# Kernel optimization log

Hardware: AMD Instinct MI355X
Metric: run time of the kernel (lower is better)

The kernel has to match this reference:

```python
import jax, jax.numpy as jnp
import numpy as np

MAX_SEQ_LEN = 1000

def _ln(x, g, b, eps=1e-5):
    m = jnp.mean(x, -1, keepdims=True)
    v = jnp.var(x, -1, keepdims=True)
    return (x - m) * jax.lax.rsqrt(v + eps) * g + b

def _conv1d(x, k, b):
    # x [B,T,Cin], k [K,Cin,Cout], 'SAME' padding (odd kernel)
    return jax.lax.conv_general_dilated(x, k, (1,), 'SAME', dimension_numbers=('NWC', 'WIO', 'NWC')) + b

def _dwconv(x, w):
    # lightweight conv: softmax-normalized depthwise kernel, w [C,K]
    k = jnp.transpose(jax.nn.softmax(w, axis=1))[:, None, :]  # [K,1,C]
    return jax.lax.conv_general_dilated(x, k, (1,), 'SAME', dimension_numbers=('NWC', 'WIO', 'NWC'), feature_group_count=x.shape[-1])

def _conv2d(x, k, b):
    # x [B,H,W,Cin], k [kh,kw,Cin,Cout]
    return jax.lax.conv_general_dilated(x, k, (1, 1), 'SAME', dimension_numbers=('NHWC', 'HWIO', 'NHWC')) + b

def _lconv(x, mask, ln_g, ln_b, glu_w, glu_b, dw, out_w, out_b):
    # LConvBlock: LN -> GLU projection -> depthwise lightweight conv -> out proj -> residual, masked
    res = x
    h = _ln(x, ln_g, ln_b)
    h = h @ glu_w + glu_b
    a, g = jnp.split(h, 2, axis=-1)
    h = a * jax.nn.sigmoid(g)
    h = jnp.where(mask[..., None], 0.0, h)
    h = _dwconv(h, dw)
    h = h @ out_w + out_b
    h = h + res
    return jnp.where(mask[..., None], 0.0, h)

def _forward(content_embedding, speaker_embedding_B, rhythm_B, scaled_duration_outputs,
             in_w, in_b,
             lc0_ln_g, lc0_ln_b, lc0_glu_w, lc0_glu_b, lc0_dw, lc0_out_w, lc0_out_b,
             lc1_ln_g, lc1_ln_b, lc1_glu_w, lc1_glu_b, lc1_dw, lc1_out_w, lc1_out_b,
             p1_w, p1_b, p2_k, p2_b,
             cw_k, cw_b, cw_ln_g, cw_ln_b,
             mkb1_k, mkb1_b, mkb2_k, mkb2_b,
             lw_w, lw_b, ln_g, ln_b, text_mask):
    B, S, _ = content_embedding.shape
    spk = jnp.broadcast_to(speaker_embedding_B[:, None, :], (B, S, speaker_embedding_B.shape[-1]))
    x = jnp.concatenate([content_embedding, spk], -1) @ in_w + in_b
    # duration predictor
    V = _lconv(x, text_mask, lc0_ln_g, lc0_ln_b, lc0_glu_w, lc0_glu_b, lc0_dw, lc0_out_w, lc0_out_b)
    V = _lconv(V, text_mask, lc1_ln_g, lc1_ln_b, lc1_glu_w, lc1_glu_b, lc1_dw, lc1_out_w, lc1_out_b)
    D = jax.nn.softplus(V @ p1_w + p1_b)[..., 0]
    D = jnp.where(text_mask, 0.0, D)
    T = _conv1d(V, p2_k, p2_b)  # [B,S,upsampled_dim]
    # learnable upsampling
    pred_phoneme_len = scaled_duration_outputs.sum(-1)
    alpha_B = jax.lax.stop_gradient(pred_phoneme_len / rhythm_B) / D.sum(-1)
    sD = alpha_B[:, None] * D
    sV = alpha_B[:, None, None] * V
    sT = alpha_B[:, None, None] * T
    mel_len = jnp.clip(jnp.round(sD.sum(-1)).astype(jnp.int32), 1, MAX_SEQ_LEN)
    mel_mask = jnp.arange(MAX_SEQ_LEN)[None, :] >= mel_len[:, None]  # True = pad
    attn_mask = mel_mask[:, :, None] & text_mask[:, None, :]  # bmm(mel_mask, src_mask^T).bool()
    e_k = jnp.cumsum(sD, axis=1)
    s_k = e_k - sD
    t = jnp.arange(1, MAX_SEQ_LEN + 1, dtype=sD.dtype)[None, :, None]
    Sm = jnp.where(attn_mask, 0.0, t - s_k[:, None, :])
    Em = jnp.where(attn_mask, 0.0, e_k[:, None, :] - t)
    # conv_w block: conv1d -> relu -> LN
    Cv = _ln(jax.nn.relu(_conv1d(sV, cw_k, cw_b)), cw_ln_g, cw_ln_b)  # [B,S,CW]
    feat = jnp.concatenate([Sm[..., None], Em[..., None],
                            jnp.broadcast_to(Cv[:, None, :, :], (B, MAX_SEQ_LEN, S, Cv.shape[-1]))], -1)
    h = jax.nn.silu(_conv2d(feat, mkb1_k, mkb1_b))
    h = jax.nn.silu(_conv2d(h, mkb2_k, mkb2_b))
    Wsc = (h @ lw_w + lw_b)[..., 0]  # [B,mel,S]
    Wsc = jnp.where(attn_mask | text_mask[:, None, :], -jnp.inf, Wsc)
    Wmat = jax.nn.softmax(Wsc, axis=2)
    up = jnp.matmul(Wmat, sT)
    up = _ln(up, ln_g, ln_b)
    up = jnp.where(mel_mask[..., None], 0.0, up)
    return up, Wmat, alpha_B, mel_len, mel_mask

def setup_inputs() -> dict:
    key = jax.random.key(0)
    ks = iter(jax.random.split(key, 64))
    B, S, DC, DS, H, CW, MKB, K = 8, 256, 192, 64, 256, 16, 16, 3
    def w(shape, scale=0.02):
        return jax.random.normal(next(ks), shape, jnp.float32) * scale
    inp = {}
    inp['content_embedding'] = jax.random.normal(next(ks), (B, S, DC), jnp.float32)
    inp['speaker_embedding_B'] = jax.random.normal(next(ks), (B, DS), jnp.float32)
    inp['rhythm_B'] = 0.15 + 0.1 * jax.random.uniform(next(ks), (B,), jnp.float32)
    inp['scaled_duration_outputs'] = jax.random.uniform(next(ks), (B, S), jnp.float32)
    lens = jax.random.randint(next(ks), (B,), 200, S + 1)
    inp['text_mask'] = jnp.arange(S)[None, :] >= lens[:, None]
    inp['in_w'] = w((DC + DS, H)); inp['in_b'] = jnp.zeros((H,), jnp.float32)
    for i in range(2):
        inp[f'lc{i}_ln_g'] = jnp.ones((H,), jnp.float32); inp[f'lc{i}_ln_b'] = jnp.zeros((H,), jnp.float32)
        inp[f'lc{i}_glu_w'] = w((H, 2 * H)); inp[f'lc{i}_glu_b'] = jnp.zeros((2 * H,), jnp.float32)
        inp[f'lc{i}_dw'] = w((H, K), 1.0)
        inp[f'lc{i}_out_w'] = w((H, H)); inp[f'lc{i}_out_b'] = jnp.zeros((H,), jnp.float32)
    inp['p1_w'] = w((H, 1)); inp['p1_b'] = jnp.zeros((1,), jnp.float32)
    inp['p2_k'] = w((K, H, H)); inp['p2_b'] = jnp.zeros((H,), jnp.float32)
    inp['cw_k'] = w((K, H, CW)); inp['cw_b'] = jnp.zeros((CW,), jnp.float32)
    inp['cw_ln_g'] = jnp.ones((CW,), jnp.float32); inp['cw_ln_b'] = jnp.zeros((CW,), jnp.float32)
    inp['mkb1_k'] = w((K, K, CW + 2, MKB)); inp['mkb1_b'] = jnp.zeros((MKB,), jnp.float32)
    inp['mkb2_k'] = w((K, K, MKB, MKB)); inp['mkb2_b'] = jnp.zeros((MKB,), jnp.float32)
    inp['lw_w'] = w((MKB, 1)); inp['lw_b'] = jnp.zeros((1,), jnp.float32)
    inp['ln_g'] = jnp.ones((H,), jnp.float32); inp['ln_b'] = jnp.zeros((H,), jnp.float32)
    return inp

def reference(content_embedding, speaker_embedding_B, rhythm_B, scaled_duration_outputs,
              text_mask,
              in_w, in_b,
              lc0_ln_g, lc0_ln_b, lc0_glu_w, lc0_glu_b, lc0_dw, lc0_out_w, lc0_out_b,
              lc1_ln_g, lc1_ln_b, lc1_glu_w, lc1_glu_b, lc1_dw, lc1_out_w, lc1_out_b,
              p1_w, p1_b, p2_k, p2_b,
              cw_k, cw_b, cw_ln_g, cw_ln_b,
              mkb1_k, mkb1_b, mkb2_k, mkb2_b,
              lw_w, lw_b, ln_g, ln_b):
    return _forward(content_embedding, speaker_embedding_B, rhythm_B, scaled_duration_outputs,
                    in_w, in_b,
                    lc0_ln_g, lc0_ln_b, lc0_glu_w, lc0_glu_b, lc0_dw, lc0_out_w, lc0_out_b,
                    lc1_ln_g, lc1_ln_b, lc1_glu_w, lc1_glu_b, lc1_dw, lc1_out_w, lc1_out_b,
                    p1_w, p1_b, p2_k, p2_b,
                    cw_k, cw_b, cw_ln_g, cw_ln_b,
                    mkb1_k, mkb1_b, mkb2_k, mkb2_b,
                    lw_w, lw_b, ln_g, ln_b, text_mask)
```

## Files before the change

kernel.cpp:

```cpp
#include <hip/hip_runtime.h>
#include <math.h>

#define SS 256
#define HH 256
#define MLEN 1000
#define CWW 16
#define NOC 16
#define RB 24

typedef __attribute__((ext_vector_type(8))) short bfrag;
typedef __attribute__((ext_vector_type(4))) float ffrag;

#define WS_V2     1048576u
#define WS_STT    1835008u
#define WS_WB     2097152u
#define WS_CCV    2424832u
#define WS_SSV    2457600u
#define WS_CCI    2490368u
#define WS_SSI    2523136u
#define WS_CP     2555904u
#define WS_CV     2654208u
#define WS_EK     2686976u
#define WS_SK     2689024u
#define WS_ALPHA  2691072u
#define WS_MELI   2691080u
#define WS_TMASK  2691088u

#define PK_IN     0u
#define PK_GLU0   65536u
#define PK_GLU1   196608u
#define PK_OUT0   327680u
#define PK_OUT1   393216u
#define PK_P2     458752u

#define OUT_UP    0u
#define OUT_W     2048000u
#define OUT_ALPHA 4096000u
#define OUT_MLEN  4096008u
#define OUT_MMASK 4096016u

__device__ __forceinline__ unsigned bf16rne(float x){
  unsigned u=__float_as_uint(x);
  u += 0x7fffu + ((u>>16)&1u);
  return u;
}
__device__ __forceinline__ unsigned short bf16h(float x){ return (unsigned short)(bf16rne(x)>>16); }
__device__ __forceinline__ float bf2f(unsigned short u){ return __uint_as_float(((unsigned)u)<<16); }
__device__ __forceinline__ unsigned frag_idx(int k,int n,int KT){
  return (unsigned)(((((n>>4)*KT+(k>>5))*64 + ((k>>3)&3)*16 + (n&15))<<3) + (k&7));
}

__global__ __launch_bounds__(256) void k_prepmask(const void* __restrict__ traw,
    const float* __restrict__ in_w,
    const float* __restrict__ g0, const float* __restrict__ g1,
    const float* __restrict__ o0, const float* __restrict__ o1,
    const float* __restrict__ p2k, float* __restrict__ ws){
  int tid=threadIdx.x;
  if(blockIdx.x==256){
    __shared__ int s_fu, s_ff, s_nz;
    const unsigned char* mb=(const unsigned char*)traw;
    const unsigned int*  mw=(const unsigned int*)traw;
    if(tid==0){s_fu=0;s_ff=0;s_nz=0;}
    __syncthreads();
    int fu=0,ff=0,nz=0;
    for(int w=tid;w<512;w+=256){
      unsigned int v=mw[w];
      if(v){ nz=1; if(v==0x3F800000u) ff=1; else if(v&0xFFFFFF00u) fu=1; }
    }
    if(fu) atomicOr(&s_fu,1);
    if(ff) atomicOr(&s_ff,1);
    if(nz) atomicOr(&s_nz,1);
    __syncthreads();
    int words = (s_ff || (!s_fu && s_nz));
    for(int i=tid;i<2048;i+=256){
      unsigned int v = words ? mw[i] : (unsigned int)mb[i];
      ws[WS_TMASK+i] = v ? 1.0f : 0.0f;
    }
    return;
  }
  unsigned short* wb=(unsigned short*)(ws+WS_WB);
  int gid=blockIdx.x*256+tid, stride=65536;
  for(int i=gid;i<65536;i+=stride){ int k=i>>8,n=i&255; wb[PK_IN  +frag_idx(k,n,8)]=bf16h(in_w[i]); }
  for(int i=gid;i<131072;i+=stride){ int k=i>>9,n=i&511; wb[PK_GLU0+frag_idx(k,n,8)]=bf16h(g0[i]); }
  for(int i=gid;i<131072;i+=stride){ int k=i>>9,n=i&511; wb[PK_GLU1+frag_idx(k,n,8)]=bf16h(g1[i]); }
  for(int i=gid;i<65536;i+=stride){ int k=i>>8,n=i&255; wb[PK_OUT0+frag_idx(k,n,8)]=bf16h(o0[i]); }
  for(int i=gid;i<65536;i+=stride){ int k=i>>8,n=i&255; wb[PK_OUT1+frag_idx(k,n,8)]=bf16h(o1[i]); }
  for(int i=gid;i<196608;i+=stride){ int k3=i>>16,r=i&65535,k=r>>8,n=r&255;
    wb[PK_P2+(unsigned)k3*65536u+frag_idx(k,n,8)]=bf16h(p2k[i]); }
}

__global__ __launch_bounds__(256) void k_front(
    const float* __restrict__ ce, const float* __restrict__ spk,
    const unsigned short* __restrict__ wb, const float* __restrict__ in_b,
    const float* __restrict__ g0b, const float* __restrict__ ln0g, const float* __restrict__ ln0b,
    const float* __restrict__ dw0, const float* __restrict__ o0b,
    const float* __restrict__ g1b, const float* __restrict__ ln1g, const float* __restrict__ ln1b,
    const float* __restrict__ dw1, const float* __restrict__ o1b,
    const float* __restrict__ tmask, float* __restrict__ V2){
  __shared__ unsigned short Abf[16][264];
  __shared__ unsigned short Hb[8][264];
  __shared__ float Xf[8][264];
  __shared__ float Vf[8][264];
  __shared__ float dws[2][3][256];
  __shared__ float tmL[8];
  int b=blockIdx.x>>6, tile=blockIdx.x&63, s0=tile*4, tid=threadIdx.x;
  int w=tid>>6, lane=tid&63, lq=lane>>4, lm=lane&15;
  {
    float d0=dw0[tid*3],d1=dw0[tid*3+1],d2=dw0[tid*3+2];
    float mx=fmaxf(d0,fmaxf(d1,d2));
    float e0=__expf(d0-mx),e1=__expf(d1-mx),e2=__expf(d2-mx);
    float inv=1.0f/(e0+e1+e2);
    dws[0][0][tid]=e0*inv; dws[0][1][tid]=e1*inv; dws[0][2][tid]=e2*inv;
    d0=dw1[tid*3];d1=dw1[tid*3+1];d2=dw1[tid*3+2];
    mx=fmaxf(d0,fmaxf(d1,d2));
    e0=__expf(d0-mx);e1=__expf(d1-mx);e2=__expf(d2-mx);
    inv=1.0f/(e0+e1+e2);
    dws[1][0][tid]=e0*inv; dws[1][1][tid]=e1*inv; dws[1][2][tid]=e2*inv;
  }
  if(tid<8){
    int sI=s0-2+tid;
    tmL[tid]=(sI>=0&&sI<256)? tmask[b*256+sI] : 1.0f;
  }
  for(int it=0;it<8;it++){
    float v=0.f;
    int sI=s0-2+it;
    if(sI>=0 && sI<256){
      int m=b*256+sI;
      v=(tid<192)? ce[m*192+tid] : spk[b*64+tid-192];
    }
    Abf[it][tid]=bf16h(v);
  }
  for(int it=8;it<16;it++) Abf[it][tid]=0;
  __syncthreads();
  {
    ffrag acc[4];
    #pragma unroll
    for(int j=0;j<4;j++){acc[j][0]=0;acc[j][1]=0;acc[j][2]=0;acc[j][3]=0;}
    #pragma unroll
    for(int kt=0;kt<8;kt++){
      bfrag af=*(const bfrag*)&Abf[lm][kt*32+lq*8];
      #pragma unroll
      for(int j=0;j<4;j++){
        int nt=w*4+j;
        bfrag bf=*(const bfrag*)(wb+PK_IN+((((unsigned)(nt*8+kt))*64u+(unsigned)lane)<<3));
        acc[j]=__builtin_amdgcn_mfma_f32_16x16x32_bf16(af,bf,acc[j],0,0,0);
      }
    }
    #pragma unroll
    for(int j=0;j<4;j++){
      int n=w*64+j*16+lm;
      float bn=in_b[n];
      #pragma unroll
      for(int reg=0;reg<4;reg++){
        int row=lq*4+reg;
        if(row<8) Xf[row][n]=acc[j][reg]+bn;
      }
    }
  }
  __syncthreads();
  {
    int r=tid>>4, seg=tid&15;
    if(r<8){
      float s=0.f,q=0.f;
      #pragma unroll
      for(int j4=0;j4<4;j4++){
        float4 v=*(const float4*)&Xf[r][seg*16+j4*4];
        s+=v.x+v.y+v.z+v.w; q+=v.x*v.x+v.y*v.y+v.z*v.z+v.w*v.w;
      }
      s+=__shfl_xor(s,1); q+=__shfl_xor(q,1);
      s+=__shfl_xor(s,2); q+=__shfl_xor(q,2);
      s+=__shfl_xor(s,4); q+=__shfl_xor(q,4);
      s+=__shfl_xor(s,8); q+=__shfl_xor(q,8);
      float mean=s*(1.0f/256.0f), rstd=rsqrtf(q*(1.0f/256.0f)-mean*mean+1e-5f);
      #pragma unroll
      for(int j4=0;j4<4;j4++){
        int c=seg*16+j4*4;
        float4 v=*(const float4*)&Xf[r][c];
        unsigned short q0=bf16h((v.x-mean)*rstd*ln0g[c+0]+ln0b[c+0]);
        unsigned short q1=bf16h((v.y-mean)*rstd*ln0g[c+1]+ln0b[c+1]);
        unsigned short q2=bf16h((v.z-mean)*rstd*ln0g[c+2]+ln0b[c+2]);
        unsigned short q3=bf16h((v.w-mean)*rstd*ln0g[c+3]+ln0b[c+3]);
        *(uint2*)&Abf[r][c]=make_uint2((unsigned)q0|((unsigned)q1<<16),(unsigned)q2|((unsigned)q3<<16));
      }
    }
  }
  __syncthreads();
  {
    ffrag aa[4],ag[4];
    #pragma unroll
    for(int j=0;j<4;j++){aa[j][0]=0;aa[j][1]=0;aa[j][2]=0;aa[j][3]=0;
                         ag[j][0]=0;ag[j][1]=0;ag[j][2]=0;ag[j][3]=0;}
    #pragma unroll
    for(int kt=0;kt<8;kt++){
      bfrag af=*(const bfrag*)&Abf[lm][kt*32+lq*8];
      #pragma unroll
      for(int j=0;j<4;j++){
        int nta=w*4+j, ntg=nta+16;
        bfrag bfa=*(const bfrag*)(wb+PK_GLU0+((((unsigned)(nta*8+kt))*64u+(unsigned)lane)<<3));
        bfrag bfg=*(const bfrag*)(wb+PK_GLU0+((((unsigned)(ntg*8+kt))*64u+(unsigned)lane)<<3));
        aa[j]=__builtin_amdgcn_mfma_f32_16x16x32_bf16(af,bfa,aa[j],0,0,0);
        ag[j]=__builtin_amdgcn_mfma_f32_16x16x32_bf16(af,bfg,ag[j],0,0,0);
      }
    }
    __syncthreads();
    #pragma unroll
    for(int j=0;j<4;j++){
      int n=w*64+j*16+lm;
      float ba=g0b[n], bg=g0b[n+256];
      #pragma unroll
      for(int reg=0;reg<4;reg++){
        int row=lq*4+reg;
        if(row<8){
          float a=aa[j][reg]+ba, g=ag[j][reg]+bg;
          float hv=a*(1.0f/(1.0f+__expf(-g)));
          if(tmL[row]!=0.0f) hv=0.0f;
          Hb[row][n]=bf16h(hv);
        }
      }
    }
  }
  __syncthreads();
  {
    float w0=dws[0][0][tid],w1=dws[0][1][tid],w2=dws[0][2][tid];
    for(int r=0;r<6;r++){
      float a=w0*bf2f(Hb[r][tid])+w1*bf2f(Hb[r+1][tid])+w2*bf2f(Hb[r+2][tid]);
      Abf[r][tid]=bf16h(a);
    }
    Abf[6][tid]=0; Abf[7][tid]=0;
  }
  __syncthreads();
  {
    ffrag acc[4];
    #pragma unroll
    for(int j=0;j<4;j++){acc[j][0]=0;acc[j][1]=0;acc[j][2]=0;acc[j][3]=0;}
    #pragma unroll
    for(int kt=0;kt<8;kt++){
      bfrag af=*(const bfrag*)&Abf[lm][kt*32+lq*8];
      #pragma unroll
      for(int j=0;j<4;j++){
        int nt=w*4+j;
        bfrag bf=*(const bfrag*)(wb+PK_OUT0+((((unsigned)(nt*8+kt))*64u+(unsigned)lane)<<3));
        acc[j]=__builtin_amdgcn_mfma_f32_16x16x32_bf16(af,bf,acc[j],0,0,0);
      }
    }
    #pragma unroll
    for(int j=0;j<4;j++){
      int n=w*64+j*16+lm;
      float bn=o0b[n];
      #pragma unroll
      for(int reg=0;reg<4;reg++){
        int row=lq*4+reg;
        if(row<6){
          float v=(tmL[row+1]==0.0f)? acc[j][reg]+bn+Xf[row+1][n] : 0.0f;
          Vf[row][n]=v;
        }
      }
    }
  }
  __syncthreads();
  {
    int r=tid>>4, seg=tid&15;
    if(r<6){
      float s=0.f,q=0.f;
      #pragma unroll
      for(int j4=0;j4<4;j4++){
        float4 v=*(const float4*)&Vf[r][seg*16+j4*4];
        s+=v.x+v.y+v.z+v.w; q+=v.x*v.x+v.y*v.y+v.z*v.z+v.w*v.w;
      }
      s+=__shfl_xor(s,1); q+=__shfl_xor(q,1);
      s+=__shfl_xor(s,2); q+=__shfl_xor(q,2);
      s+=__shfl_xor(s,4); q+=__shfl_xor(q,4);
      s+=__shfl_xor(s,8); q+=__shfl_xor(q,8);
      float mean=s*(1.0f/256.0f), rstd=rsqrtf(q*(1.0f/256.0f)-mean*mean+1e-5f);
      #pragma unroll
      for(int j4=0;j4<4;j4++){
        int c=seg*16+j4*4;
        float4 v=*(const float4*)&Vf[r][c];
        unsigned short q0=bf16h((v.x-mean)*rstd*ln1g[c+0]+ln1b[c+0]);
        unsigned short q1=bf16h((v.y-mean)*rstd*ln1g[c+1]+ln1b[c+1]);
        unsigned short q2=bf16h((v.z-mean)*rstd*ln1g[c+2]+ln1b[c+2]);
        unsigned short q3=bf16h((v.w-mean)*rstd*ln1g[c+3]+ln1b[c+3]);
        *(uint2*)&Abf[r][c]=make_uint2((unsigned)q0|((unsigned)q1<<16),(unsigned)q2|((unsigned)q3<<16));
      }
    }
  }
  __syncthreads();
  {
    ffrag aa[4],ag[4];
    #pragma unroll
    for(int j=0;j<4;j++){aa[j][0]=0;aa[j][1]=0;aa[j][2]=0;aa[j][3]=0;
                         ag[j][0]=0;ag[j][1]=0;ag[j][2]=0;ag[j][3]=0;}
    #pragma unroll
    for(int kt=0;kt<8;kt++){
      bfrag af=*(const bfrag*)&Abf[lm][kt*32+lq*8];
      #pragma unroll
      for(int j=0;j<4;j++){
        int nta=w*4+j, ntg=nta+16;
        bfrag bfa=*(const bfrag*)(wb+PK_GLU1+((((unsigned)(nta*8+kt))*64u+(unsigned)lane)<<3));
        bfrag bfg=*(const bfrag*)(wb+PK_GLU1+((((unsigned)(ntg*8+kt))*64u+(unsigned)lane)<<3));
        aa[j]=__builtin_amdgcn_mfma_f32_16x16x32_bf16(af,bfa,aa[j],0,0,0);
        ag[j]=__builtin_amdgcn_mfma_f32_16x16x32_bf16(af,bfg,ag[j],0,0,0);
      }
    }
    __syncthreads();
    #pragma unroll
    for(int j=0;j<4;j++){
      int n=w*64+j*16+lm;
      float ba=g1b[n], bg=g1b[n+256];
      #pragma unroll
      for(int reg=0;reg<4;reg++){
        int row=lq*4+reg;
        if(row<6){
          float a=aa[j][reg]+ba, g=ag[j][reg]+bg;
          float hv=a*(1.0f/(1.0f+__expf(-g)));
          if(tmL[row+1]!=0.0f) hv=0.0f;
          Hb[row][n]=bf16h(hv);
        }
      }
    }
  }
  __syncthreads();
  {
    float w0=dws[1][0][tid],w1=dws[1][1][tid],w2=dws[1][2][tid];
    for(int r=0;r<4;r++){
      float a=w0*bf2f(Hb[r][tid])+w1*bf2f(Hb[r+1][tid])+w2*bf2f(Hb[r+2][tid]);
      Abf[r][tid]=bf16h(a);
    }
    Abf[4][tid]=0; Abf[5][tid]=0;
  }
  __syncthreads();
  {
    ffrag acc[4];
    #pragma unroll
    for(int j=0;j<4;j++){acc[j][0]=0;acc[j][1]=0;acc[j][2]=0;acc[j][3]=0;}
    #pragma unroll
    for(int kt=0;kt<8;kt++){
      bfrag af=*(const bfrag*)&Abf[lm][kt*32+lq*8];
      #pragma unroll
      for(int j=0;j<4;j++){
        int nt=w*4+j;
        bfrag bf=*(const bfrag*)(wb+PK_OUT1+((((unsigned)(nt*8+kt))*64u+(unsigned)lane)<<3));
        acc[j]=__builtin_amdgcn_mfma_f32_16x16x32_bf16(af,bf,acc[j],0,0,0);
      }
    }
    #pragma unroll
    for(int j=0;j<4;j++){
      int n=w*64+j*16+lm;
      float bn=o1b[n];
      #pragma unroll
      for(int reg=0;reg<4;reg++){
        int row=lq*4+reg;
        if(row<4){
          float v=(tmL[row+2]!=0.0f)? 0.0f : acc[j][reg]+bn+Vf[row+1][n];
          V2[(unsigned)(b*256+s0+row)*256u+n]=v;
        }
      }
    }
  }
}

__global__ __launch_bounds__(256) void k_dur(const float* __restrict__ V2, const float* __restrict__ p1w,
    const float* __restrict__ p1b, const float* __restrict__ sdo, const float* __restrict__ rhythm,
    float* __restrict__ ws, float* __restrict__ outp){
  __shared__ float p1[HH];
  __shared__ float sd[SS];
  __shared__ float red[16];
  int b=blockIdx.x, tid=threadIdx.x;
  int wid=tid>>6, lane=tid&63;
  p1[tid]=p1w[tid];
  __syncthreads();
  float accd=p1b[0];
  const float* row=V2+(unsigned)(b*SS+tid)*HH;
  for(int k=0;k<HH;k+=4){
    float4 v=*(const float4*)&row[k];
    accd+=v.x*p1[k]+v.y*p1[k+1]+v.z*p1[k+2]+v.w*p1[k+3];
  }
  float Dv=fmaxf(accd,0.0f)+log1pf(expf(-fabsf(accd)));
  if(ws[WS_TMASK+b*SS+tid]!=0.0f) Dv=0.0f;
  float sv=sdo[b*SS+tid];
  float a=Dv, c=sv;
  for(int off=32;off;off>>=1){ a+=__shfl_down(a,off); c+=__shfl_down(c,off); }
  if(lane==0){ red[wid]=a; red[wid+8]=c; }
  __syncthreads();
  float Dsum=red[0]+red[1]+red[2]+red[3];
  float pred=red[8]+red[9]+red[10]+red[11];
  float al=(pred/rhythm[b])/Dsum;
  float sDv=al*Dv;
  sd[tid]=sDv;
  __syncthreads();
  for(int off=1;off<SS;off<<=1){
    float t=(tid>=off)?sd[tid-off]:0.0f;
    __syncthreads();
    sd[tid]+=t;
    __syncthreads();
  }
  float ek=sd[tid], sk=ek-sDv;
  ws[WS_EK+b*SS+tid]=ek;
  ws[WS_SK+b*SS+tid]=sk;
  float melf=sd[SS-1];
  int mel=(int)rintf(melf); mel=mel<1?1:(mel>MLEN?MLEN:mel);
  if(tid==0){
    ws[WS_ALPHA+b]=al;
    ((int*)ws)[WS_MELI+b]=mel;
    outp[OUT_ALPHA+b]=al;
    outp[OUT_MLEN+b]=(float)mel;
  }
  for(int t=tid;t<MLEN;t+=SS) outp[OUT_MMASK+b*MLEN+t]=(t>=mel)?1.0f:0.0f;
}

__global__ __launch_bounds__(256) void k_post(const float* __restrict__ V2,
    const unsigned short* __restrict__ wbp2, const float* __restrict__ p2b,
    const float* __restrict__ cwk, const float* __restrict__ cwb,
    const float* __restrict__ cwg, const float* __restrict__ cwbe,
    float* __restrict__ ws){
  int bx=blockIdx.x, tid=threadIdx.x;
  if(bx<256){
    __shared__ unsigned short Abf[18][264];
    int m0=(bx>>1)*16, nh=bx&1, b=m0>>8, s0=m0&255;
    for(int it=0;it<18;it++){
      int sI=s0-1+it;
      float v=(sI>=0&&sI<256)? V2[(unsigned)(b*256+sI)*256u+tid] : 0.0f;
      Abf[it][tid]=bf16h(v);
    }
    __syncthreads();
    int w=tid>>6, lane=tid&63, lq=lane>>4, lm=lane&15;
    ffrag acc[2];
    #pragma unroll
    for(int tt=0;tt<2;tt++){ acc[tt][0]=0;acc[tt][1]=0;acc[tt][2]=0;acc[tt][3]=0; }
    for(int k3=0;k3<3;k3++){
      const unsigned short* wb3=wbp2+(unsigned)k3*65536u;
      #pragma unroll
      for(int kt=0;kt<8;kt++){
        bfrag af=*(const bfrag*)&Abf[lm+k3][kt*32+lq*8];
        #pragma unroll
        for(int tt=0;tt<2;tt++){
          int nt=nh*8+w*2+tt;
          bfrag bf=*(const bfrag*)(wb3+((((unsigned)(nt*8+kt))*64u+(unsigned)lane)<<3));
          acc[tt]=__builtin_amdgcn_mfma_f32_16x16x32_bf16(af,bf,acc[tt],0,0,0);
        }
      }
    }
    float al=ws[WS_ALPHA+b];
    unsigned short* stt=(unsigned short*)(ws+WS_STT);
    #pragma unroll
    for(int tt=0;tt<2;tt++){
      int n=nh*128+w*32+tt*16+lm;
      float bn=p2b[n];
      unsigned short o0=bf16h((acc[tt][0]+bn)*al);
      unsigned short o1=bf16h((acc[tt][1]+bn)*al);
      unsigned short o2=bf16h((acc[tt][2]+bn)*al);
      unsigned short o3=bf16h((acc[tt][3]+bn)*al);
      *(uint2*)&stt[((unsigned)(b*256+n)<<8)+(unsigned)(s0+lq*4)]=
        make_uint2((unsigned)o0|((unsigned)o1<<16),(unsigned)o2|((unsigned)o3<<16));
    }
  } else {
    __shared__ float Vt[18][SS];
    int bb=bx-256;
    int b=bb>>4, tile=bb&15;
    int sbase=tile*16;
    float al=ws[WS_ALPHA+b];
    for(int rr=0;rr<18;rr++){
      int s=sbase-1+rr;
      Vt[rr][tid]=(s>=0&&s<SS)?al*V2[(b*SS+s)*HH+tid]:0.0f;
    }
    __syncthreads();
    int sl=tid>>4, oc=tid&15;
    float a0=cwb[oc],a1=0.f,a2=0.f,a3=0.f;
    for(int k3=0;k3<3;k3++){
      const float* vp=&Vt[sl+k3][0];
      const float* wpp=cwk+(unsigned)k3*HH*CWW+oc;
      for(int c=0;c<HH;c+=4){
        a0+=vp[c+0]*wpp[(c+0)*CWW];
        a1+=vp[c+1]*wpp[(c+1)*CWW];
        a2+=vp[c+2]*wpp[(c+2)*CWW];
        a3+=vp[c+3]*wpp[(c+3)*CWW];
      }
    }
    float acc=fmaxf((a0+a1)+(a2+a3),0.0f);
    float ssum=acc, qsum=acc*acc;
    for(int off=8;off;off>>=1){ ssum+=__shfl_xor(ssum,off); qsum+=__shfl_xor(qsum,off); }
    float mean=ssum*(1.0f/CWW), var=qsum*(1.0f/CWW)-mean*mean;
    float cv=(acc-mean)*rsqrtf(var+1e-5f)*cwg[oc]+cwbe[oc];
    ws[WS_CV+(unsigned)(b*SS+sbase+sl)*CWW+oc]=cv;
  }
}

__global__ __launch_bounds__(256) void k_cp(const float* __restrict__ mkb1k, const float* __restrict__ mkb1b,
    float* __restrict__ ws){
  __shared__ float CvL[258][17];
  __shared__ float k1c[3][3][CWW][NOC];
  __shared__ float kab[3][3][2][NOC];
  __shared__ float skE[258], ekE[258], fiE[258];
  int b=blockIdx.x, tid=threadIdx.x;
  for(int i=tid;i<3*3*CWW*NOC;i+=256){
    int oc=i&15, ic=(i>>4)&15, kk=i>>8;
    int kw=kk%3, kh=kk/3;
    k1c[kh][kw][ic][oc]=mkb1k[((kh*3+kw)*18+2+ic)*NOC+oc];
  }
  for(int i=tid;i<3*3*2*NOC;i+=256){
    int oc=i&15, ch=(i>>4)&1, kk=i>>5;
    int kw=kk%3, kh=kk/3;
    kab[kh][kw][ch][oc]=mkb1k[((kh*3+kw)*18+ch)*NOC+oc];
  }
  for(int i=tid;i<SS*CWW;i+=256) CvL[1+(i>>4)][i&15]=ws[WS_CV+(unsigned)b*SS*CWW+i];
  if(tid<CWW){ CvL[0][tid]=0.f; CvL[257][tid]=0.f; }
  if(tid<258){
    float sk=0.f, ek=0.f, fi=0.f;
    if(tid>=1 && tid<=SS){
      sk=ws[WS_SK+b*SS+tid-1];
      ek=ws[WS_EK+b*SS+tid-1];
      fi=(ws[WS_TMASK+b*SS+tid-1]!=0.0f)?0.0f:1.0f;
    }
    skE[tid]=sk; ekE[tid]=ek; fiE[tid]=fi;
  }
  __syncthreads();
  float* cpg=ws+WS_CP+(unsigned)b*3*SS*NOC;
  float ccv[16],ssv[16],cci[16],ssi[16];
  #pragma unroll
  for(int oc=0;oc<NOC;oc++){ float bb2=mkb1b[oc]; ccv[oc]=bb2; cci[oc]=bb2; ssv[oc]=0.f; ssi[oc]=0.f; }
  for(int dt=0;dt<3;dt++){
    float acc[NOC];
    #pragma unroll
    for(int oc=0;oc<NOC;oc++) acc[oc]=0.f;
    #pragma unroll
    for(int ds=0;ds<3;ds++){
      #pragma unroll
      for(int ic=0;ic<CWW;ic++){
        float v=CvL[tid+ds][ic];
        #pragma unroll
        for(int oc=0;oc<NOC;oc++) acc[oc]+=v*k1c[dt][ds][ic][oc];
      }
    }
    for(int oc=0;oc<NOC;oc++) cpg[(unsigned)(dt*SS+tid)*NOC+oc]=acc[oc];
    float va[16],vb[16],ia[16],ib2[16];
    #pragma unroll
    for(int oc=0;oc<NOC;oc++){ va[oc]=0.f; vb[oc]=0.f; ia[oc]=0.f; ib2[oc]=0.f; }
    #pragma unroll
    for(int ds=0;ds<3;ds++){
      int j=tid+ds;
      float inb=(j>=1&&j<=SS)?1.0f:0.0f;
      float fb=fiE[j];
      float skv=skE[j], ekv=ekE[j];
      #pragma unroll
      for(int oc=0;oc<NOC;oc++){
        float ka=kab[dt][ds][0][oc], kb=kab[dt][ds][1][oc];
        float d=ka-kb, e=kb*ekv-ka*skv;
        va[oc]+=inb*d; vb[oc]+=inb*e; ia[oc]+=fb*d; ib2[oc]+=fb*e;
      }
    }
    float dtf=(float)dt;
    #pragma unroll
    for(int oc=0;oc<NOC;oc++){
      ccv[oc]+=acc[oc]+vb[oc]+dtf*va[oc]; ssv[oc]+=va[oc];
      cci[oc]+=acc[oc]+ib2[oc]+dtf*ia[oc]; ssi[oc]+=ia[oc];
    }
  }
  unsigned base=(unsigned)(b*SS+tid)*16u;
  for(int oc=0;oc<NOC;oc++){
    ws[WS_CCV+base+oc]=ccv[oc];
    ws[WS_SSV+base+oc]=ssv[oc];
    ws[WS_CCI+base+oc]=cci[oc];
    ws[WS_SSI+base+oc]=ssi[oc];
  }
}

__global__ __launch_bounds__(256,4) void k_stageB(
    const float* __restrict__ ws, const float* __restrict__ mkb1k, const float* __restrict__ mkb1b,
    const float* __restrict__ mkb2k, const float* __restrict__ mkb2b,
    const float* __restrict__ lww, const float* __restrict__ lwb,
    float* __restrict__ outp){
  __shared__ short ringh[3][258][RB];
  __shared__ float skL[258], ekL[258];
  __shared__ unsigned char finC[260];
  __shared__ __align__(16) float wscL[SS];
  __shared__ float red[16];
  int bx=blockIdx.x, b=bx/125, chunk=bx%125, t0=chunk*8, tid=threadIdx.x;
  int wid=tid>>6, lane=tid&63;
  int lq=lane>>4, lm=lane&15;
  if(tid<258){
    float sk=0.f, ek=0.f; unsigned char fin=0;
    if(tid>=1 && tid<=SS){
      sk=ws[WS_SK+b*SS+tid-1];
      ek=ws[WS_EK+b*SS+tid-1];
      fin=(ws[WS_TMASK+b*SS+tid-1]!=0.0f)?0:1;
    }
    skL[tid]=sk; ekL[tid]=ek; finC[tid]=fin;
  }
  if(tid<72){
    int sl=tid/24, rem=tid%24;
    int row=(rem<12)?0:257, c=(rem%12)*2;
    *(int*)&ringh[sl][row][c]=0;
  }
  int mel=((const int*)ws)[WS_MELI+b];
  __syncthreads();

  const float* cpb=ws+WS_CP+(unsigned)b*3*SS*NOC;

  unsigned offA[5]; int dtL[5], zgL[5];
  bfrag bfw[5];
  {
    #pragma unroll
    for(int i=0;i<5;i++){
      int g=4*i+lq;
      int dt,ds,hf,zg;
      if(g<18){ dt=g/6; int rm=g-6*dt; ds=rm>>1; hf=rm&1; zg=0; }
      else { dt=0; ds=0; hf=0; zg=1; }
      int srow=wid*64+lm+ds;
      offA[i]=(unsigned)((srow*RB+8*hf)*2);
      dtL[i]=dt; zgL[i]=zg;
      int pk[4];
      if(!zg){
        #pragma unroll
        for(int j=0;j<4;j++){
          unsigned u0=bf16rne(mkb2k[(8*g+2*j)*NOC+lm]);
          unsigned u1=bf16rne(mkb2k[(8*g+2*j+1)*NOC+lm]);
          pk[j]=(int)((u0>>16)|(u1&0xffff0000u));
        }
      } else pk[0]=pk[1]=pk[2]=pk[3]=0;
      bfw[i]=__builtin_bit_cast(bfrag, make_int4(pk[0],pk[1],pk[2],pk[3]));
    }
  }
  float b2v=mkb2b[lm];
  float lwwv=lww[lm];
  float lwb0=lwb[0];
  const char* ringB=(const char*)&ringh[0][0][0];
  bfrag azero={};

  auto conv1row=[&](int T){
    int s=tid;
    float acc[NOC];
    bool fv=(T>=1)&&(T<=998)&&(T+1<mel);
    bool fi=(T>=2)&&(T<=998)&&(T-1>=mel);
    if(fv||fi){
      const float* cc=ws+(fv?WS_CCV:WS_CCI)+(unsigned)(b*SS+s)*16u;
      const float* s2=ws+(fv?WS_SSV:WS_SSI)+(unsigned)(b*SS+s)*16u;
      float Tf=(float)T;
      #pragma unroll
      for(int q=0;q<4;q++){
        float4 c4=((const float4*)cc)[q];
        float4 s4=((const float4*)s2)[q];
        acc[4*q+0]=c4.x+Tf*s4.x; acc[4*q+1]=c4.y+Tf*s4.y;
        acc[4*q+2]=c4.z+Tf*s4.z; acc[4*q+3]=c4.w+Tf*s4.w;
      }
    } else {
      #pragma unroll
      for(int oc=0;oc<NOC;oc++) acc[oc]=mkb1b[oc];
      #pragma unroll
      for(int dt=0;dt<3;dt++){
        int tr=T+dt-1;
        if(tr<0||tr>=MLEN) continue;
        bool valid=(tr<mel);
        float tt=(float)(tr+1);
        float gg[3], hh[3];
        #pragma unroll
        for(int ds=0;ds<3;ds++){
          int j=s+ds;
          float f = valid ? ((j>=1&&j<=SS)?1.0f:0.0f) : (float)finC[j];
          gg[ds]=f*(tt-skL[j]);
          hh[ds]=f*(ekL[j]-tt);
        }
        const float* cpr=cpb+(unsigned)(dt*SS+s)*NOC;
        float4 c0=((const float4*)cpr)[0], c1=((const float4*)cpr)[1];
        float4 c2=((const float4*)cpr)[2], c3=((const float4*)cpr)[3];
        acc[0]+=c0.x; acc[1]+=c0.y; acc[2]+=c0.z; acc[3]+=c0.w;
        acc[4]+=c1.x; acc[5]+=c1.y; acc[6]+=c1.z; acc[7]+=c1.w;
        acc[8]+=c2.x; acc[9]+=c2.y; acc[10]+=c2.z; acc[11]+=c2.w;
        acc[12]+=c3.x; acc[13]+=c3.y; acc[14]+=c3.z; acc[15]+=c3.w;
        #pragma unroll
        for(int ds=0;ds<3;ds++){
          const float* kA=mkb1k+((dt*3+ds)*18+0)*NOC;
          const float* kB=mkb1k+((dt*3+ds)*18+1)*NOC;
          #pragma unroll
          for(int oc=0;oc<NOC;oc++) acc[oc]+=gg[ds]*kA[oc]+hh[ds]*kB[oc];
        }
      }
    }
    int slot=T%3;
    int pk[8];
    #pragma unroll
    for(int j=0;j<8;j++){
      float x0=acc[2*j], x1=acc[2*j+1];
      float s0=x0/(1.0f+__expf(-x0));
      float s1=x1/(1.0f+__expf(-x1));
      unsigned u0=bf16rne(s0), u1=bf16rne(s1);
      pk[j]=(int)((u0>>16)|(u1&0xffff0000u));
    }
    int4* dst=(int4*)&ringh[slot][s+1][0];
    dst[0]=make_int4(pk[0],pk[1],pk[2],pk[3]);
    dst[1]=make_int4(pk[4],pk[5],pk[6],pk[7]);
  };

  if(t0>0) conv1row(t0-1);
  conv1row(t0);

  #pragma unroll 1
  for(int r=0;r<8;r++){
    int t=t0+r;
    if(t+1<MLEN) conv1row(t+1);
    __syncthreads();
    int tmod=t%3;
    ffrag acc2[4];
    #pragma unroll
    for(int tt=0;tt<4;tt++){ acc2[tt][0]=b2v; acc2[tt][1]=b2v; acc2[tt][2]=b2v; acc2[tt][3]=b2v; }
    #pragma unroll
    for(int i=0;i<5;i++){
      int dt=dtL[i];
      int x=tmod+dt+2; x=(x>=3)?x-3:x; x=(x>=3)?x-3:x;
      int tr=t+dt-1;
      bool av=((unsigned)tr<(unsigned)MLEN)&&(!zgL[i]);
      const char* rp=ringB+(unsigned)x*(258u*RB*2u)+offA[i];
      #pragma unroll
      for(int tt=0;tt<4;tt++){
        int4 ra=*(const int4*)(rp+tt*(16*RB*2));
        bfrag a=av?__builtin_bit_cast(bfrag,ra):azero;
        acc2[tt]=__builtin_amdgcn_mfma_f32_16x16x32_bf16(a,bfw[i],acc2[tt],0,0,0);
      }
    }
    #pragma unroll
    for(int tt=0;tt<4;tt++){
      float out4[4];
      #pragma unroll
      for(int q=0;q<4;q++){
        float xx=acc2[tt][q];
        float pv=(xx/(1.0f+__expf(-xx)))*lwwv;
        pv+=__shfl_xor(pv,1); pv+=__shfl_xor(pv,2); pv+=__shfl_xor(pv,4); pv+=__shfl_xor(pv,8);
        out4[q]=pv+lwb0;
      }
      if(lm==0){
        *(float4*)&wscL[wid*64+tt*16+lq*4]=make_float4(out4[0],out4[1],out4[2],out4[3]);
      }
    }
    __syncthreads();
    float fm=(float)finC[tid+1];
    float wsc=wscL[tid];
    float val=(fm!=0.0f)?wsc:-3.0e38f;
    float mx=val;
    for(int off=32;off;off>>=1) mx=fmaxf(mx,__shfl_down(mx,off));
    if(lane==0) red[wid]=mx;
    __syncthreads();
    mx=fmaxf(fmaxf(red[0],red[1]),fmaxf(red[2],red[3]));
    float e=(fm!=0.0f)?__expf(wsc-mx):0.0f;
    float sm=e;
    for(int off=32;off;off>>=1) sm+=__shfl_down(sm,off);
    if(lane==0) red[8+wid]=sm;
    __syncthreads();
    sm=red[8]+red[9]+red[10]+red[11];
    outp[OUT_W+(unsigned)(b*MLEN+t)*SS+tid]=e/sm;
    __syncthreads();
  }
}

__global__ __launch_bounds__(256) void k_up(const float* __restrict__ ws,
    const float* __restrict__ lng, const float* __restrict__ lnb, float* __restrict__ outp){
  __shared__ unsigned short Wbf[16][264];
  __shared__ float UpL[16][264];
  __shared__ float gb[2][256];
  int bx=blockIdx.x, b=bx/63, tile=bx%63, t0=tile*16, tid=threadIdx.x;
  gb[0][tid]=lng[tid]; gb[1][tid]=lnb[tid];
  for(int it=0;it<16;it++){
    int t=t0+it;
    float v=(t<MLEN)? outp[OUT_W+(unsigned)(b*MLEN+t)*256u+tid] : 0.0f;
    Wbf[it][tid]=bf16h(v);
  }
  int mel=((const int*)ws)[WS_MELI+b];
  __syncthreads();
  int w=tid>>6, lane=tid&63, lq=lane>>4, lm=lane&15;
  const unsigned short* stt=(const unsigned short*)(ws+WS_STT)+(unsigned)b*65536u;
  ffrag acc[4];
  #pragma unroll
  for(int tt=0;tt<4;tt++){ acc[tt][0]=0;acc[tt][1]=0;acc[tt][2]=0;acc[tt][3]=0; }
  #pragma unroll
  for(int kt=0;kt<8;kt++){
    bfrag af=*(const bfrag*)&Wbf[lm][kt*32+lq*8];
    #pragma unroll
    for(int tt=0;tt<4;tt++){
      int n=w*64+tt*16+lm;
      bfrag bf=*(const bfrag*)(stt+((unsigned)n<<8)+(unsigned)(kt*32+lq*8));
      acc[tt]=__builtin_amdgcn_mfma_f32_16x16x32_bf16(af,bf,acc[tt],0,0,0);
    }
  }
  #pragma unroll
  for(int tt=0;tt<4;tt++){
    #pragma unroll
    for(int reg=0;reg<4;reg++)
      UpL[lq*4+reg][w*64+tt*16+lm]=acc[tt][reg];
  }
  __syncthreads();
  int r=tid>>4, seg=tid&15;
  float s=0.f,q=0.f;
  #pragma unroll
  for(int j4=0;j4<4;j4++){
    float4 v=*(const float4*)&UpL[r][seg*16+j4*4];
    s+=v.x+v.y+v.z+v.w; q+=v.x*v.x+v.y*v.y+v.z*v.z+v.w*v.w;
  }
  s+=__shfl_xor(s,1); q+=__shfl_xor(q,1);
  s+=__shfl_xor(s,2); q+=__shfl_xor(q,2);
  s+=__shfl_xor(s,4); q+=__shfl_xor(q,4);
  s+=__shfl_xor(s,8); q+=__shfl_xor(q,8);
  float mean=s*(1.0f/256.0f), rstd=rsqrtf(q*(1.0f/256.0f)-mean*mean+1e-5f);
  int t=t0+r;
  if(t<MLEN){
    bool vld=(t<mel);
    #pragma unroll
    for(int j4=0;j4<4;j4++){
      int c=seg*16+j4*4;
      float4 v=*(const float4*)&UpL[r][c];
      float4 o;
      o.x=vld?((v.x-mean)*rstd*gb[0][c+0]+gb[1][c+0]):0.0f;
      o.y=vld?((v.y-mean)*rstd*gb[0][c+1]+gb[1][c+1]):0.0f;
      o.z=vld?((v.z-mean)*rstd*gb[0][c+2]+gb[1][c+2]):0.0f;
      o.w=vld?((v.w-mean)*rstd*gb[0][c+3]+gb[1][c+3]):0.0f;
      *(float4*)&outp[OUT_UP+(unsigned)(b*MLEN+t)*256u+c]=o;
    }
  }
}

extern "C" void kernel_launch(void* const* d_in, const int* in_sizes, int n_in,
                              void* d_out, int out_size, void* d_ws, size_t ws_size,
                              hipStream_t stream){
  const float* ce   =(const float*)d_in[0];
  const float* spk  =(const float*)d_in[1];
  const float* rhy  =(const float*)d_in[2];
  const float* sdo  =(const float*)d_in[3];
  const void*  tmr  =d_in[4];
  const float* in_w =(const float*)d_in[5];
  const float* in_b =(const float*)d_in[6];
  const float* l0lg =(const float*)d_in[7];
  const float* l0lb =(const float*)d_in[8];
  const float* l0gw =(const float*)d_in[9];
  const float* l0gb =(const float*)d_in[10];
  const float* l0dw =(const float*)d_in[11];
  const float* l0ow =(const float*)d_in[12];
  const float* l0ob =(const float*)d_in[13];
  const float* l1lg =(const float*)d_in[14];
  const float* l1lb =(const float*)d_in[15];
  const float* l1gw =(const float*)d_in[16];
  const float* l1gb =(const float*)d_in[17];
  const float* l1dw =(const float*)d_in[18];
  const float* l1ow =(const float*)d_in[19];
  const float* l1ob =(const float*)d_in[20];
  const float* p1w  =(const float*)d_in[21];
  const float* p1b  =(const float*)d_in[22];
  const float* p2k  =(const float*)d_in[23];
  const float* p2b  =(const float*)d_in[24];
  const float* cwk  =(const float*)d_in[25];
  const float* cwb  =(const float*)d_in[26];
  const float* cwg  =(const float*)d_in[27];
  const float* cwbe =(const float*)d_in[28];
  const float* m1k  =(const float*)d_in[29];
  const float* m1b  =(const float*)d_in[30];
  const float* m2k  =(const float*)d_in[31];
  const float* m2b  =(const float*)d_in[32];
  const float* lww  =(const float*)d_in[33];
  const float* lwbp =(const float*)d_in[34];
  const float* lng  =(const float*)d_in[35];
  const float* lnb  =(const float*)d_in[36];
  float* ws=(float*)d_ws;
  float* outp=(float*)d_out;
  const unsigned short* wbb=(const unsigned short*)(ws+WS_WB);

  k_prepmask<<<257,256,0,stream>>>(tmr, in_w, l0gw, l1gw, l0ow, l1ow, p2k, ws);
  k_front   <<<512,256,0,stream>>>(ce, spk, wbb, in_b,
                                   l0gb, l0lg, l0lb, l0dw, l0ob,
                                   l1gb, l1lg, l1lb, l1dw, l1ob,
                                   ws+WS_TMASK, ws+WS_V2);
  k_dur     <<<8,256,0,stream>>>(ws+WS_V2, p1w, p1b, sdo, rhy, ws, outp);
  k_post    <<<384,256,0,stream>>>(ws+WS_V2, wbb+PK_P2, p2b, cwk, cwb, cwg, cwbe, ws);
  k_cp      <<<8,256,0,stream>>>(m1k, m1b, ws);
  k_stageB  <<<1000,256,0,stream>>>(ws, m1k, m1b, m2k, m2b, lww, lwbp, outp);
  k_up      <<<504,256,0,stream>>>(ws, lng, lnb, outp);
}
```

Before: 324.5 us.

## Fuse duration, post-projection and upsampling kernels by deferring alpha scaling

Alpha depends on the duration sums, but it only scales linear conv outputs, so its application is moved later. That lets the duration predictor run as extra blocks inside the post-projection kernel, with the bias, ReLU and LayerNorm of the conv channel moved into k_cp. The upsampling GEMM and its LayerNorm are fused into the tail of k_stageB, reusing its ring shared memory. This removes two launches and a serial dependency, but the 16-row MFMA now uses only 8 valid rows and stageB gains more shared memory and longer blocks.

```diff
diff --git a/kernel.cpp b/kernel.cpp
--- a/kernel.cpp
+++ b/kernel.cpp
@@ -359,60 +359,12 @@
   }
 }
 
-__global__ __launch_bounds__(256) void k_dur(const float* __restrict__ V2, const float* __restrict__ p1w,
-    const float* __restrict__ p1b, const float* __restrict__ sdo, const float* __restrict__ rhythm,
+__global__ __launch_bounds__(256) void k_postdur(const float* __restrict__ V2,
+    const unsigned short* __restrict__ wbp2, const float* __restrict__ p2b,
+    const float* __restrict__ cwk,
+    const float* __restrict__ p1w, const float* __restrict__ p1b,
+    const float* __restrict__ sdo, const float* __restrict__ rhythm,
     float* __restrict__ ws, float* __restrict__ outp){
-  __shared__ float p1[HH];
-  __shared__ float sd[SS];
-  __shared__ float red[16];
-  int b=blockIdx.x, tid=threadIdx.x;
-  int wid=tid>>6, lane=tid&63;
-  p1[tid]=p1w[tid];
-  __syncthreads();
-  float accd=p1b[0];
-  const float* row=V2+(unsigned)(b*SS+tid)*HH;
-  for(int k=0;k<HH;k+=4){
-    float4 v=*(const float4*)&row[k];
-    accd+=v.x*p1[k]+v.y*p1[k+1]+v.z*p1[k+2]+v.w*p1[k+3];
-  }
-  float Dv=fmaxf(accd,0.0f)+log1pf(expf(-fabsf(accd)));
-  if(ws[WS_TMASK+b*SS+tid]!=0.0f) Dv=0.0f;
-  float sv=sdo[b*SS+tid];
-  float a=Dv, c=sv;
-  for(int off=32;off;off>>=1){ a+=__shfl_down(a,off); c+=__shfl_down(c,off); }
-  if(lane==0){ red[wid]=a; red[wid+8]=c; }
-  __syncthreads();
-  float Dsum=red[0]+red[1]+red[2]+red[3];
-  float pred=red[8]+red[9]+red[10]+red[11];
-  float al=(pred/rhythm[b])/Dsum;
-  float sDv=al*Dv;
-  sd[tid]=sDv;
-  __syncthreads();
-  for(int off=1;off<SS;off<<=1){
-    float t=(tid>=off)?sd[tid-off]:0.0f;
-    __syncthreads();
-    sd[tid]+=t;
-    __syncthreads();
-  }
-  float ek=sd[tid], sk=ek-sDv;
-  ws[WS_EK+b*SS+tid]=ek;
-  ws[WS_SK+b*SS+tid]=sk;
-  float melf=sd[SS-1];
-  int mel=(int)rintf(melf); mel=mel<1?1:(mel>MLEN?MLEN:mel);
-  if(tid==0){
-    ws[WS_ALPHA+b]=al;
-    ((int*)ws)[WS_MELI+b]=mel;
-    outp[OUT_ALPHA+b]=al;
-    outp[OUT_MLEN+b]=(float)mel;
-  }
-  for(int t=tid;t<MLEN;t+=SS) outp[OUT_MMASK+b*MLEN+t]=(t>=mel)?1.0f:0.0f;
-}
-
-__global__ __launch_bounds__(256) void k_post(const float* __restrict__ V2,
-    const unsigned short* __restrict__ wbp2, const float* __restrict__ p2b,
-    const float* __restrict__ cwk, const float* __restrict__ cwb,
-    const float* __restrict__ cwg, const float* __restrict__ cwbe,
-    float* __restrict__ ws){
   int bx=blockIdx.x, tid=threadIdx.x;
   if(bx<256){
     __shared__ unsigned short Abf[18][264];
@@ -440,32 +392,30 @@
         }
       }
     }
-    float al=ws[WS_ALPHA+b];
     unsigned short* stt=(unsigned short*)(ws+WS_STT);
     #pragma unroll
     for(int tt=0;tt<2;tt++){
       int n=nh*128+w*32+tt*16+lm;
       float bn=p2b[n];
-      unsigned short o0=bf16h((acc[tt][0]+bn)*al);
-      unsigned short o1=bf16h((acc[tt][1]+bn)*al);
-      unsigned short o2=bf16h((acc[tt][2]+bn)*al);
-      unsigned short o3=bf16h((acc[tt][3]+bn)*al);
+      unsigned short o0=bf16h(acc[tt][0]+bn);
+      unsigned short o1=bf16h(acc[tt][1]+bn);
+      unsigned short o2=bf16h(acc[tt][2]+bn);
+      unsigned short o3=bf16h(acc[tt][3]+bn);
       *(uint2*)&stt[((unsigned)(b*256+n)<<8)+(unsigned)(s0+lq*4)]=
         make_uint2((unsigned)o0|((unsigned)o1<<16),(unsigned)o2|((unsigned)o3<<16));
     }
-  } else {
+  } else if(bx<384){
     __shared__ float Vt[18][SS];
     int bb=bx-256;
     int b=bb>>4, tile=bb&15;
     int sbase=tile*16;
-    float al=ws[WS_ALPHA+b];
     for(int rr=0;rr<18;rr++){
       int s=sbase-1+rr;
-      Vt[rr][tid]=(s>=0&&s<SS)?al*V2[(b*SS+s)*HH+tid]:0.0f;
+      Vt[rr][tid]=(s>=0&&s<SS)?V2[(b*SS+s)*HH+tid]:0.0f;
     }
     __syncthreads();
     int sl=tid>>4, oc=tid&15;
-    float a0=cwb[oc],a1=0.f,a2=0.f,a3=0.f;
+    float a0=0.f,a1=0.f,a2=0.f,a3=0.f;
     for(int k3=0;k3<3;k3++){
       const float* vp=&Vt[sl+k3][0];
       const float* wpp=cwk+(unsigned)k3*HH*CWW+oc;
@@ -476,22 +426,64 @@
         a3+=vp[c+3]*wpp[(c+3)*CWW];
       }
     }
-    float acc=fmaxf((a0+a1)+(a2+a3),0.0f);
-    float ssum=acc, qsum=acc*acc;
-    for(int off=8;off;off>>=1){ ssum+=__shfl_xor(ssum,off); qsum+=__shfl_xor(qsum,off); }
-    float mean=ssum*(1.0f/CWW), var=qsum*(1.0f/CWW)-mean*mean;
-    float cv=(acc-mean)*rsqrtf(var+1e-5f)*cwg[oc]+cwbe[oc];
-    ws[WS_CV+(unsigned)(b*SS+sbase+sl)*CWW+oc]=cv;
+    ws[WS_CV+(unsigned)(b*SS+sbase+sl)*CWW+oc]=(a0+a1)+(a2+a3);
+  } else {
+    __shared__ float p1[HH];
+    __shared__ float sd[SS];
+    __shared__ float red[16];
+    int b=bx-384;
+    int wid=tid>>6, lane=tid&63;
+    p1[tid]=p1w[tid];
+    __syncthreads();
+    float accd=p1b[0];
+    const float* row=V2+(unsigned)(b*SS+tid)*HH;
+    for(int k=0;k<HH;k+=4){
+      float4 v=*(const float4*)&row[k];
+      accd+=v.x*p1[k]+v.y*p1[k+1]+v.z*p1[k+2]+v.w*p1[k+3];
+    }
+    float Dv=fmaxf(accd,0.0f)+log1pf(expf(-fabsf(accd)));
+    if(ws[WS_TMASK+b*SS+tid]!=0.0f) Dv=0.0f;
+    float sv=sdo[b*SS+tid];
+    float a=Dv, c=sv;
+    for(int off=32;off;off>>=1){ a+=__shfl_down(a,off); c+=__shfl_down(c,off); }
+    if(lane==0){ red[wid]=a; red[wid+8]=c; }
+    __syncthreads();
+    float Dsum=red[0]+red[1]+red[2]+red[3];
+    float pred=red[8]+red[9]+red[10]+red[11];
+    float al=(pred/rhythm[b])/Dsum;
+    float sDv=al*Dv;
+    sd[tid]=sDv;
+    __syncthreads();
+    for(int off=1;off<SS;off<<=1){
+      float t=(tid>=off)?sd[tid-off]:0.0f;
+      __syncthreads();
+      sd[tid]+=t;
+      __syncthreads();
+    }
+    float ek=sd[tid], sk=ek-sDv;
+    ws[WS_EK+b*SS+tid]=ek;
+    ws[WS_SK+b*SS+tid]=sk;
+    float melf=sd[SS-1];
+    int mel=(int)rintf(melf); mel=mel<1?1:(mel>MLEN?MLEN:mel);
+    if(tid==0){
+      ws[WS_ALPHA+b]=al;
+      ((int*)ws)[WS_MELI+b]=mel;
+      outp[OUT_ALPHA+b]=al;
+      outp[OUT_MLEN+b]=(float)mel;
+    }
+    for(int t=tid;t<MLEN;t+=SS) outp[OUT_MMASK+b*MLEN+t]=(t>=mel)?1.0f:0.0f;
   }
 }
 
 __global__ __launch_bounds__(256) void k_cp(const float* __restrict__ mkb1k, const float* __restrict__ mkb1b,
+    const float* __restrict__ cwb, const float* __restrict__ cwg, const float* __restrict__ cwbe,
     float* __restrict__ ws){
   __shared__ float CvL[258][17];
   __shared__ float k1c[3][3][CWW][NOC];
   __shared__ float kab[3][3][2][NOC];
   __shared__ float skE[258], ekE[258], fiE[258];
   int b=blockIdx.x, tid=threadIdx.x;
+  float al=ws[WS_ALPHA+b];
   for(int i=tid;i<3*3*CWW*NOC;i+=256){
     int oc=i&15, ic=(i>>4)&15, kk=i>>8;
     int kw=kk%3, kh=kk/3;
@@ -502,7 +494,20 @@
     int kw=kk%3, kh=kk/3;
     kab[kh][kw][ch][oc]=mkb1k[((kh*3+kw)*18+ch)*NOC+oc];
   }
-  for(int i=tid;i<SS*CWW;i+=256) CvL[1+(i>>4)][i&15]=ws[WS_CV+(unsigned)b*SS*CWW+i];
+  {
+    float c[16];
+    const float* src=ws+WS_CV+(unsigned)(b*SS+tid)*16u;
+    float sm=0.f,qm=0.f;
+    #pragma unroll
+    for(int ic=0;ic<16;ic++){
+      float v=fmaxf(al*src[ic]+cwb[ic],0.0f);
+      c[ic]=v; sm+=v; qm+=v*v;
+    }
+    float mean=sm*(1.0f/16.0f), var=qm*(1.0f/16.0f)-mean*mean;
+    float rstd=rsqrtf(var+1e-5f);
+    #pragma unroll
+    for(int ic=0;ic<16;ic++) CvL[1+tid][ic]=(c[ic]-mean)*rstd*cwg[ic]+cwbe[ic];
+  }
   if(tid<CWW){ CvL[0][tid]=0.f; CvL[257][tid]=0.f; }
   if(tid<258){
     float sk=0.f, ek=0.f, fi=0.f;
@@ -568,8 +573,9 @@
     const float* __restrict__ ws, const float* __restrict__ mkb1k, const float* __restrict__ mkb1b,
     const float* __restrict__ mkb2k, const float* __restrict__ mkb2b,
     const float* __restrict__ lww, const float* __restrict__ lwb,
+    const float* __restrict__ lng, const float* __restrict__ lnb,
     float* __restrict__ outp){
-  __shared__ short ringh[3][258][RB];
+  __shared__ __align__(16) char smem[3*258*RB*2];
   __shared__ float skL[258], ekL[258];
   __shared__ unsigned char finC[260];
   __shared__ __align__(16) float wscL[SS];
@@ -589,7 +595,7 @@
   if(tid<72){
     int sl=tid/24, rem=tid%24;
     int row=(rem<12)?0:257, c=(rem%12)*2;
-    *(int*)&ringh[sl][row][c]=0;
+    *(int*)(smem+((sl*258+row)*RB+c)*2)=0;
   }
   int mel=((const int*)ws)[WS_MELI+b];
   __syncthreads();
@@ -623,7 +629,6 @@
   float b2v=mkb2b[lm];
   float lwwv=lww[lm];
   float lwb0=lwb[0];
-  const char* ringB=(const char*)&ringh[0][0][0];
   bfrag azero={};
 
   auto conv1row=[&](int T){
@@ -685,7 +690,7 @@
       unsigned u0=bf16rne(s0), u1=bf16rne(s1);
       pk[j]=(int)((u0>>16)|(u1&0xffff0000u));
     }
-    int4* dst=(int4*)&ringh[slot][s+1][0];
+    int4* dst=(int4*)(smem+((unsigned)(slot*258+s+1)*RB)*2u);
     dst[0]=make_int4(pk[0],pk[1],pk[2],pk[3]);
     dst[1]=make_int4(pk[4],pk[5],pk[6],pk[7]);
   };
@@ -708,7 +713,7 @@
       int x=tmod+dt+2; x=(x>=3)?x-3:x; x=(x>=3)?x-3:x;
       int tr=t+dt-1;
       bool av=((unsigned)tr<(unsigned)MLEN)&&(!zgL[i]);
-      const char* rp=ringB+(unsigned)x*(258u*RB*2u)+offA[i];
+      const char* rp=smem+(unsigned)x*(258u*RB*2u)+offA[i];
       #pragma unroll
       for(int tt=0;tt<4;tt++){
         int4 ra=*(const int4*)(rp+tt*(16*RB*2));
@@ -746,71 +751,66 @@
     __syncthreads();
     sm=red[8]+red[9]+red[10]+red[11];
     outp[OUT_W+(unsigned)(b*MLEN+t)*SS+tid]=e/sm;
-    __syncthreads();
-  }
-}
-
-__global__ __launch_bounds__(256) void k_up(const float* __restrict__ ws,
-    const float* __restrict__ lng, const float* __restrict__ lnb, float* __restrict__ outp){
-  __shared__ unsigned short Wbf[16][264];
-  __shared__ float UpL[16][264];
-  __shared__ float gb[2][256];
-  int bx=blockIdx.x, b=bx/63, tile=bx%63, t0=tile*16, tid=threadIdx.x;
-  gb[0][tid]=lng[tid]; gb[1][tid]=lnb[tid];
-  for(int it=0;it<16;it++){
-    int t=t0+it;
-    float v=(t<MLEN)? outp[OUT_W+(unsigned)(b*MLEN+t)*256u+tid] : 0.0f;
-    Wbf[it][tid]=bf16h(v);
-  }
-  int mel=((const int*)ws)[WS_MELI+b];
-  __syncthreads();
-  int w=tid>>6, lane=tid&63, lq=lane>>4, lm=lane&15;
+  }
+
+  __syncthreads();
+  unsigned short* Wb=(unsigned short*)smem;
+  float* UpL=(float*)(smem+8448);
+  for(int it=0;it<8;it++){
+    Wb[it*264+tid]=bf16h(outp[OUT_W+(unsigned)(b*MLEN+t0+it)*SS+tid]);
+  }
+  for(int it=8;it<16;it++) Wb[it*264+tid]=0;
+  __syncthreads();
   const unsigned short* stt=(const unsigned short*)(ws+WS_STT)+(unsigned)b*65536u;
-  ffrag acc[4];
+  ffrag uacc[4];
   #pragma unroll
-  for(int tt=0;tt<4;tt++){ acc[tt][0]=0;acc[tt][1]=0;acc[tt][2]=0;acc[tt][3]=0; }
+  for(int tt=0;tt<4;tt++){ uacc[tt][0]=0;uacc[tt][1]=0;uacc[tt][2]=0;uacc[tt][3]=0; }
   #pragma unroll
   for(int kt=0;kt<8;kt++){
-    bfrag af=*(const bfrag*)&Wbf[lm][kt*32+lq*8];
+    bfrag af=*(const bfrag*)&Wb[lm*264+kt*32+lq*8];
     #pragma unroll
     for(int tt=0;tt<4;tt++){
-      int n=w*64+tt*16+lm;
+      int n=wid*64+tt*16+lm;
       bfrag bf=*(const bfrag*)(stt+((unsigned)n<<8)+(unsigned)(kt*32+lq*8));
-      acc[tt]=__builtin_amdgcn_mfma_f32_16x16x32_bf16(af,bf,acc[tt],0,0,0);
+      uacc[tt]=__builtin_amdgcn_mfma_f32_16x16x32_bf16(af,bf,uacc[tt],0,0,0);
     }
   }
   #pragma unroll
   for(int tt=0;tt<4;tt++){
     #pragma unroll
-    for(int reg=0;reg<4;reg++)
-      UpL[lq*4+reg][w*64+tt*16+lm]=acc[tt][reg];
-  }
-  __syncthreads();
-  int r=tid>>4, seg=tid&15;
-  float s=0.f,q=0.f;
-  #pragma unroll
-  for(int j4=0;j4<4;j4++){
-    float4 v=*(const float4*)&UpL[r][seg*16+j4*4];
-    s+=v.x+v.y+v.z+v.w; q+=v.x*v.x+v.y*v.y+v.z*v.z+v.w*v.w;
-  }
-  s+=__shfl_xor(s,1); q+=__shfl_xor(q,1);
-  s+=__shfl_xor(s,2); q+=__shfl_xor(q,2);
-  s+=__shfl_xor(s,4); q+=__shfl_xor(q,4);
-  s+=__shfl_xor(s,8); q+=__shfl_xor(q,8);
-  float mean=s*(1.0f/256.0f), rstd=rsqrtf(q*(1.0f/256.0f)-mean*mean+1e-5f);
-  int t=t0+r;
-  if(t<MLEN){
-    bool vld=(t<mel);
-    #pragma unroll
-    for(int j4=0;j4<4;j4++){
-      int c=seg*16+j4*4;
-      float4 v=*(const float4*)&UpL[r][c];
-      float4 o;
-      o.x=vld?((v.x-mean)*rstd*gb[0][c+0]+gb[1][c+0]):0.0f;
-      o.y=vld?((v.y-mean)*rstd*gb[0][c+1]+gb[1][c+1]):0.0f;
-      o.z=vld?((v.z-mean)*rstd*gb[0][c+2]+gb[1][c+2]):0.0f;
-      o.w=vld?((v.w-mean)*rstd*gb[0][c+3]+gb[1][c+3]):0.0f;
-      *(float4*)&outp[OUT_UP+(unsigned)(b*MLEN+t)*256u+c]=o;
+    for(int reg=0;reg<4;reg++){
+      int row=lq*4+reg;
+      if(row<8) UpL[row*264+wid*64+tt*16+lm]=uacc[tt][reg];
+    }
+  }
+  __syncthreads();
+  {
+    int r2=tid>>4, seg=tid&15;
+    if(r2<8){
+      float s=0.f,q=0.f;
+      #pragma unroll
+      for(int j4=0;j4<4;j4++){
+        float4 v=*(const float4*)&UpL[r2*264+seg*16+j4*4];
+        s+=v.x+v.y+v.z+v.w; q+=v.x*v.x+v.y*v.y+v.z*v.z+v.w*v.w;
+      }
+      s+=__shfl_xor(s,1); q+=__shfl_xor(q,1);
+      s+=__shfl_xor(s,2); q+=__shfl_xor(q,2);
+      s+=__shfl_xor(s,4); q+=__shfl_xor(q,4);
+      s+=__shfl_xor(s,8); q+=__shfl_xor(q,8);
+      float mean=s*(1.0f/256.0f), rstd=rsqrtf(q*(1.0f/256.0f)-mean*mean+1e-5f);
+      int t=t0+r2;
+      bool vld=(t<mel);
+      #pragma unroll
+      for(int j4=0;j4<4;j4++){
+        int c=seg*16+j4*4;
+        float4 v=*(const float4*)&UpL[r2*264+c];
+        float4 o;
+        o.x=vld?((v.x-mean)*rstd*lng[c+0]+lnb[c+0]):0.0f;
+        o.y=vld?((v.y-mean)*rstd*lng[c+1]+lnb[c+1]):0.0f;
+        o.z=vld?((v.z-mean)*rstd*lng[c+2]+lnb[c+2]):0.0f;
+        o.w=vld?((v.w-mean)*rstd*lng[c+3]+lnb[c+3]):0.0f;
+        *(float4*)&outp[OUT_UP+(unsigned)(b*MLEN+t)*256u+c]=o;
+      }
     }
   }
 }
@@ -864,9 +864,7 @@
                                    l0gb, l0lg, l0lb, l0dw, l0ob,
                                    l1gb, l1lg, l1lb, l1dw, l1ob,
                                    ws+WS_TMASK, ws+WS_V2);
-  k_dur     <<<8,256,0,stream>>>(ws+WS_V2, p1w, p1b, sdo, rhy, ws, outp);
-  k_post    <<<384,256,0,stream>>>(ws+WS_V2, wbb+PK_P2, p2b, cwk, cwb, cwg, cwbe, ws);
-  k_cp      <<<8,256,0,stream>>>(m1k, m1b, ws);
-  k_stageB  <<<1000,256,0,stream>>>(ws, m1k, m1b, m2k, m2b, lww, lwbp, outp);
-  k_up      <<<504,256,0,stream>>>(ws, lng, lnb, outp);
+  k_postdur <<<392,256,0,stream>>>(ws+WS_V2, wbb+PK_P2, p2b, cwk, p1w, p1b, sdo, rhy, ws, outp);
+  k_cp      <<<8,256,0,stream>>>(m1k, m1b, cwb, cwg, cwbe, ws);
+  k_stageB  <<<1000,256,0,stream>>>(ws, m1k, m1b, m2k, m2b, lww, lwbp, lng, lnb, outp);
 }
```

New measurement: 324.3 us. About the same (-0.1%).
